# Performance work log

Hardware: AMD Instinct MI355X
Metric: run time of the kernel (lower is better)

## Reference

```python
import jax, jax.numpy as jnp
import numpy as np

NOISE_EPS = 0.01
TOP_K = 2


def setup_inputs() -> dict:
    key = jax.random.key(0)
    k1, k2, k3, k4 = jax.random.split(key, 4)
    B, S, D, E = 4, 4096, 2048, 64
    x = jax.random.normal(k1, (B, S, D), dtype=jnp.float32)
    raw_noise = jax.random.normal(k2, (B, S, E), dtype=jnp.float32)
    # gating_mlp: single Linear(D -> E), init std=0.02, zero bias
    W_gate = 0.02 * jax.random.normal(k3, (E, D), dtype=jnp.float32)
    b_gate = jnp.zeros((E,), dtype=jnp.float32)
    # noise_projection: Linear(D -> E, bias=False), init std=1/sqrt(D)
    W_noise = (1.0 / np.sqrt(D)) * jax.random.normal(k4, (E, D), dtype=jnp.float32)
    return {"x": x, "raw_noise": raw_noise, "W_gate": W_gate, "b_gate": b_gate, "W_noise": W_noise}


def reference(x, raw_noise, W_gate, b_gate, W_noise):
    # gate logits: [B,S,E]
    logits = jnp.einsum("bsd,ed->bse", x, W_gate) + b_gate
    # noisy top-k routing (training path)
    noise_stddev = jax.nn.softplus(jnp.einsum("bsd,ed->bse", x, W_noise)) + NOISE_EPS
    noisy = logits + raw_noise * noise_stddev
    top_v, top_i = jax.lax.top_k(noisy, TOP_K)            # [B,S,K]
    top_p = jax.nn.softmax(top_v.astype(jnp.float32), axis=-1).astype(noisy.dtype)
    B, S, E = noisy.shape
    T = B * S
    flat_logits = noisy.reshape(T, E)
    flat_i = top_i.reshape(T, TOP_K)
    flat_p = top_p.reshape(T, TOP_K)
    sparse = jnp.zeros((T, E), dtype=noisy.dtype).at[jnp.arange(T)[:, None], flat_i].set(flat_p)
    # aux load-balancing loss
    indicator = (sparse > 0.0).astype(jnp.float32)
    fraction_routed = indicator.sum(axis=0) / T           # f_e
    router_probs = jax.nn.softmax(flat_logits.astype(jnp.float32), axis=-1)
    avg_prob = router_probs.mean(axis=0)                  # p_e
    aux_loss = jnp.sum(fraction_routed * avg_prob) * E
    return sparse.reshape(B, S, E), aux_loss.astype(noisy.dtype)
```

## Files before the change

### kernel.cpp

```cpp
#include <hip/hip_runtime.h>
#include <math.h>

#define TOK 16384
#define DD  2048
#define EE  64
#define MT  32
#define BK  32
#define NKC 32
#define LDA 40

typedef _Float16 half4v __attribute__((ext_vector_type(4)));
typedef _Float16 half8  __attribute__((ext_vector_type(8)));
typedef float    floatx4 __attribute__((ext_vector_type(4)));

__global__ void build_wf(const float* __restrict__ Wg, const float* __restrict__ Wn,
                         _Float16* __restrict__ wf) {
  int tid  = blockIdx.x * 256 + threadIdx.x;
  int lane = tid & 63;
  int kc   = (tid >> 6) & 63;
  int ct   = tid >> 12;
  int col  = (ct & 3) * 16 + (lane & 15);
  int k    = kc * 32 + (lane >> 4) * 8;
  const float* W = (ct < 4) ? Wg : Wn;
  const float* src = W + (size_t)col * DD + k;
  float4 a = *reinterpret_cast<const float4*>(src);
  float4 b = *reinterpret_cast<const float4*>(src + 4);
  float v[8] = {a.x, a.y, a.z, a.w, b.x, b.y, b.z, b.w};
  half8 hi, lo;
#pragma unroll
  for (int j = 0; j < 8; ++j) {
    _Float16 h = (_Float16)v[j];
    hi[j] = h;
    lo[j] = (_Float16)(v[j] - (float)h);
  }
  size_t base = (((size_t)(ct * 64 + kc) * 2 + 0) * 64 + lane) * 8;
  *reinterpret_cast<half8*>(wf + base)       = hi;
  *reinterpret_cast<half8*>(wf + base + 512) = lo;
}

__global__ __launch_bounds__(512, 4)
void gating_kernel(const float* __restrict__ x, const float* __restrict__ rn,
                   const _Float16* __restrict__ wf, const float* __restrict__ bg,
                   float* __restrict__ out,
                   float* __restrict__ cnt_g, float* __restrict__ psum_g) {
  __shared__ char smem[33920];
  _Float16* xs   = (_Float16*)smem;
  float*    Pacc = (float*)smem;
  float*    Vb   = (float*)(smem + 16384);
  float*    Eb   = (float*)(smem + 24832);
  float*    isum = (float*)(smem + 33280);
  int*      ti   = (int*)(smem + 33408);
  float*    tp   = (float*)(smem + 33664);

  const int t  = threadIdx.x;
  const int g  = t >> 8;
  const int tg = t & 255;
  const int w4 = tg >> 6;
  const int l  = t & 63;
  const int q  = l >> 4;
  const int cl = l & 15;
  const int c  = w4 * 16 + cl;
  const int t0 = blockIdx.x * MT;

  const int stok = tg >> 3;
  const int skof = (tg & 7) * 4;
  const float* xrow = x + (size_t)(t0 + stok) * DD + g * (NKC * BK) + skof;

  float bgv = 0.f;
  float rnv[2][4] = {{0.f,0.f,0.f,0.f},{0.f,0.f,0.f,0.f}};
  if (g == 0) {
    bgv = bg[c];
#pragma unroll
    for (int mt = 0; mt < 2; ++mt)
#pragma unroll
      for (int r = 0; r < 4; ++r)
        rnv[mt][r] = rn[(size_t)(t0 + mt * 16 + q * 4 + r) * EE + c];
  }

  floatx4 acc[2][2];
#pragma unroll
  for (int mt = 0; mt < 2; ++mt)
#pragma unroll
    for (int nt = 0; nt < 2; ++nt) acc[mt][nt] = (floatx4)0.f;

  const half8* wfp = (const half8*)wf;
  half8 B[2][2][2];

  {
    float4 a = *reinterpret_cast<const float4*>(xrow);
    float v[4] = {a.x, a.y, a.z, a.w};
    half4v hi, lo;
#pragma unroll
    for (int j = 0; j < 4; ++j) {
      _Float16 h = (_Float16)v[j];
      hi[j] = h;
      lo[j] = (_Float16)(v[j] - (float)h);
    }
    *reinterpret_cast<half4v*>(&xs[((g * 2 + 0) * 2 + 0) * (MT * LDA) + stok * LDA + skof]) = hi;
    *reinterpret_cast<half4v*>(&xs[((g * 2 + 0) * 2 + 1) * (MT * LDA) + stok * LDA + skof]) = lo;
#pragma unroll
    for (int nt = 0; nt < 2; ++nt) {
      const int ct = w4 + nt * 4;
#pragma unroll
      for (int s = 0; s < 2; ++s)
        B[0][nt][s] = wfp[((size_t)(ct * 64 + g * NKC) * 2 + s) * 64 + l];
    }
  }

#pragma unroll 4
  for (int kc = 0; kc < NKC; ++kc) {
    const int cur = kc & 1;
    const bool more = (kc < NKC - 1);
    float4 pa;
    if (more) {
      pa = *reinterpret_cast<const float4*>(xrow + (kc + 1) * BK);
#pragma unroll
      for (int nt = 0; nt < 2; ++nt) {
        const int ct = w4 + nt * 4;
#pragma unroll
        for (int s = 0; s < 2; ++s)
          B[cur ^ 1][nt][s] = wfp[((size_t)(ct * 64 + g * NKC + kc + 1) * 2 + s) * 64 + l];
      }
    }
    asm volatile("s_waitcnt lgkmcnt(0)" ::: "memory");
    __builtin_amdgcn_s_barrier();

    half8 Ah[2], Al[2];
#pragma unroll
    for (int mt = 0; mt < 2; ++mt) {
      Ah[mt] = *reinterpret_cast<const half8*>(
          &xs[((g * 2 + cur) * 2 + 0) * (MT * LDA) + (mt * 16 + cl) * LDA + q * 8]);
      Al[mt] = *reinterpret_cast<const half8*>(
          &xs[((g * 2 + cur) * 2 + 1) * (MT * LDA) + (mt * 16 + cl) * LDA + q * 8]);
    }
#pragma unroll
    for (int mt = 0; mt < 2; ++mt)
#pragma unroll
      for (int nt = 0; nt < 2; ++nt)
        acc[mt][nt] = __builtin_amdgcn_mfma_f32_16x16x32_f16(Ah[mt], B[cur][nt][0], acc[mt][nt], 0, 0, 0);
#pragma unroll
    for (int mt = 0; mt < 2; ++mt)
#pragma unroll
      for (int nt = 0; nt < 2; ++nt)
        acc[mt][nt] = __builtin_amdgcn_mfma_f32_16x16x32_f16(Ah[mt], B[cur][nt][1], acc[mt][nt], 0, 0, 0);
#pragma unroll
    for (int mt = 0; mt < 2; ++mt)
#pragma unroll
      for (int nt = 0; nt < 2; ++nt)
        acc[mt][nt] = __builtin_amdgcn_mfma_f32_16x16x32_f16(Al[mt], B[cur][nt][0], acc[mt][nt], 0, 0, 0);

    if (more) {
      float v[4] = {pa.x, pa.y, pa.z, pa.w};
      half4v hi, lo;
#pragma unroll
      for (int j = 0; j < 4; ++j) {
        _Float16 h = (_Float16)v[j];
        hi[j] = h;
        lo[j] = (_Float16)(v[j] - (float)h);
      }
      *reinterpret_cast<half4v*>(&xs[((g * 2 + (cur ^ 1)) * 2 + 0) * (MT * LDA) + stok * LDA + skof]) = hi;
      *reinterpret_cast<half4v*>(&xs[((g * 2 + (cur ^ 1)) * 2 + 1) * (MT * LDA) + stok * LDA + skof]) = lo;
    }
  }

  __syncthreads();

  if (g == 1) {
#pragma unroll
    for (int mt = 0; mt < 2; ++mt)
#pragma unroll
      for (int nt = 0; nt < 2; ++nt)
#pragma unroll
        for (int r = 0; r < 4; ++r)
          Pacc[((((w4 * 2 + mt) * 2 + nt) * 4) + r) * 64 + l] = acc[mt][nt][r];
  }
  __syncthreads();

  if (g == 0) {
#pragma unroll
    for (int mt = 0; mt < 2; ++mt)
#pragma unroll
      for (int nt = 0; nt < 2; ++nt)
#pragma unroll
        for (int r = 0; r < 4; ++r)
          acc[mt][nt][r] += Pacc[((((w4 * 2 + mt) * 2 + nt) * 4) + r) * 64 + l];

#pragma unroll
    for (int mt = 0; mt < 2; ++mt)
#pragma unroll
      for (int r = 0; r < 4; ++r) {
        const int tk = mt * 16 + q * 4 + r;
        float gt = acc[mt][0][r] + bgv;
        float h  = acc[mt][1][r];
        float sp = (h > 20.f) ? h : log1pf(expf(h));
        float v  = gt + rnv[mt][r] * (sp + 0.01f);
        Vb[tk * 66 + c] = v;
        Eb[tk * 66 + c] = expf(v);
      }
  }
  __syncthreads();

  if (t < MT) {
    float v1 = -1e30f, v2 = -1e30f;
    int   i1 = 0, i2 = 0;
    float s = 0.f;
    for (int e = 0; e < EE; ++e) {
      float v = Vb[t * 66 + e];
      s += Eb[t * 66 + e];
      if (v > v1)      { v2 = v1; i2 = i1; v1 = v; i1 = e; }
      else if (v > v2) { v2 = v;  i2 = e; }
    }
    isum[t] = 1.f / s;
    ti[t * 2 + 0] = i1; ti[t * 2 + 1] = i2;
    float e2 = expf(v2 - v1);
    float dn = 1.f + e2;
    tp[t * 2 + 0] = 1.f / dn;
    tp[t * 2 + 1] = e2 / dn;
  }
  __syncthreads();

  {
    const int m  = t >> 4;
    const int c0 = (t & 15) * 4;
    const int i1 = ti[m * 2 + 0], i2 = ti[m * 2 + 1];
    const float p1 = tp[m * 2 + 0], p2 = tp[m * 2 + 1];
    float o[4];
#pragma unroll
    for (int j = 0; j < 4; ++j) {
      const int col = c0 + j;
      o[j] = (col == i1) ? p1 : ((col == i2) ? p2 : 0.f);
    }
    *reinterpret_cast<float4*>(out + (size_t)(t0 + m) * EE + c0) =
        make_float4(o[0], o[1], o[2], o[3]);
  }

  if (t < EE) {
    float s = 0.f;
    int   cn = 0;
#pragma unroll
    for (int m = 0; m < MT; ++m) {
      s  += Eb[m * 66 + t] * isum[m];
      cn += (ti[m * 2 + 0] == t) + (ti[m * 2 + 1] == t);
    }
    atomicAdd(&psum_g[t], s);
    atomicAdd(&cnt_g[t], (float)cn);
  }
}

__global__ void aux_kernel(const float* __restrict__ cnt_g,
                           const float* __restrict__ psum_g,
                           float* __restrict__ out) {
  int e = threadIdx.x;
  float v = cnt_g[e] * psum_g[e];
#pragma unroll
  for (int o = 32; o > 0; o >>= 1) v += __shfl_down(v, o);
  if (e == 0)
    out[(size_t)TOK * EE] = v * ((float)EE / ((float)TOK * (float)TOK));
}

extern "C" void kernel_launch(void* const* d_in, const int* in_sizes, int n_in,
                              void* d_out, int out_size, void* d_ws, size_t ws_size,
                              hipStream_t stream) {
  const float* x  = (const float*)d_in[0];
  const float* rn = (const float*)d_in[1];
  const float* Wg = (const float*)d_in[2];
  const float* bg = (const float*)d_in[3];
  const float* Wn = (const float*)d_in[4];
  float* out    = (float*)d_out;
  float* cnt_g  = (float*)d_ws;
  float* psum_g = cnt_g + EE;
  _Float16* wf  = (_Float16*)((float*)d_ws + 128);

  hipMemsetAsync(d_ws, 0, 2 * EE * sizeof(float), stream);
  build_wf<<<128, 256, 0, stream>>>(Wg, Wn, wf);
  gating_kernel<<<TOK / MT, 512, 0, stream>>>(x, rn, wf, bg, out, cnt_g, psum_g);
  aux_kernel<<<1, 64, 0, stream>>>(cnt_g, psum_g, out);
}
```

Measured before the change: 237.5 us.

## Stage four K-slices per barrier to cut synchronization in gating GEMM

Each outer iteration now stages a 128-wide K chunk of x (four 32-wide slices) into shared memory instead of one 32-wide slice, so there are 8 barriers per half-K instead of 32. Weight fragments are software-pipelined one sub-slice ahead with ping-pong registers, and more x loads are in flight per thread. Shared memory grows to about 68 KB per block, which can lower the number of resident blocks per CU and reduce occupancy.

```diff
diff --git a/kernel.cpp b/kernel.cpp
--- a/kernel.cpp
+++ b/kernel.cpp
@@ -5,9 +5,10 @@
 #define DD  2048
 #define EE  64
 #define MT  32
-#define BK  32
-#define NKC 32
-#define LDA 40
+#define BK  128
+#define NKC 8
+#define LDA 136
+#define XREG (MT * LDA)
 
 typedef _Float16 half4v __attribute__((ext_vector_type(4)));
 typedef _Float16 half8  __attribute__((ext_vector_type(8)));
@@ -38,12 +39,67 @@
   *reinterpret_cast<half8*>(wf + base + 512) = lo;
 }
 
+#define STAGE(BUF, P0, P1, P2, P3)                                              \
+  {                                                                             \
+    float4 pav[4] = {P0, P1, P2, P3};                                           \
+    _Float16* xh = xs + ((g * 2 + (BUF)) * 2 + 0) * XREG + stok * LDA + skof;   \
+    _Float16* xl = xh + XREG;                                                   \
+    _Pragma("unroll")                                                           \
+    for (int j = 0; j < 4; ++j) {                                               \
+      float v[4] = {pav[j].x, pav[j].y, pav[j].z, pav[j].w};                    \
+      half4v hi, lo;                                                            \
+      _Pragma("unroll")                                                         \
+      for (int jj = 0; jj < 4; ++jj) {                                          \
+        _Float16 h = (_Float16)v[jj];                                           \
+        hi[jj] = h;                                                             \
+        lo[jj] = (_Float16)(v[jj] - (float)h);                                  \
+      }                                                                         \
+      *reinterpret_cast<half4v*>(xh + j * 32) = hi;                             \
+      *reinterpret_cast<half4v*>(xl + j * 32) = lo;                             \
+    }                                                                           \
+  }
+
+#define SUBK(KK, SC, SP, DOPF)                                                  \
+  {                                                                             \
+    half8 Ah[2], Al[2];                                                         \
+    _Pragma("unroll")                                                           \
+    for (int mt = 0; mt < 2; ++mt) {                                            \
+      Ah[mt] = *reinterpret_cast<const half8*>(xsh + (mt * 16) * LDA + (KK) * 32); \
+      Al[mt] = *reinterpret_cast<const half8*>(xsl + (mt * 16) * LDA + (KK) * 32); \
+    }                                                                           \
+    if (DOPF) {                                                                 \
+      const int ck = g * 32 + kc * 4 + (KK) + 1;                                \
+      _Pragma("unroll")                                                         \
+      for (int nt = 0; nt < 2; ++nt) {                                          \
+        const int ct = w4 + nt * 4;                                             \
+        _Pragma("unroll")                                                       \
+        for (int s = 0; s < 2; ++s)                                             \
+          SP[nt][s] = wfp[((size_t)(ct * 64 + ck) * 2 + s) * 64 + l];           \
+      }                                                                         \
+    }                                                                           \
+    _Pragma("unroll")                                                           \
+    for (int mt = 0; mt < 2; ++mt)                                              \
+      _Pragma("unroll")                                                         \
+      for (int nt = 0; nt < 2; ++nt)                                            \
+        acc[mt][nt] = __builtin_amdgcn_mfma_f32_16x16x32_f16(Ah[mt], SC[nt][0], acc[mt][nt], 0, 0, 0); \
+    _Pragma("unroll")                                                           \
+    for (int mt = 0; mt < 2; ++mt)                                              \
+      _Pragma("unroll")                                                         \
+      for (int nt = 0; nt < 2; ++nt)                                            \
+        acc[mt][nt] = __builtin_amdgcn_mfma_f32_16x16x32_f16(Ah[mt], SC[nt][1], acc[mt][nt], 0, 0, 0); \
+    _Pragma("unroll")                                                           \
+    for (int mt = 0; mt < 2; ++mt)                                              \
+      _Pragma("unroll")                                                         \
+      for (int nt = 0; nt < 2; ++nt)                                            \
+        acc[mt][nt] = __builtin_amdgcn_mfma_f32_16x16x32_f16(Al[mt], SC[nt][0], acc[mt][nt], 0, 0, 0); \
+  }
+
 __global__ __launch_bounds__(512, 4)
 void gating_kernel(const float* __restrict__ x, const float* __restrict__ rn,
                    const _Float16* __restrict__ wf, const float* __restrict__ bg,
                    float* __restrict__ out,
                    float* __restrict__ cnt_g, float* __restrict__ psum_g) {
-  __shared__ char smem[33920];
+  __shared__ char smem[69632];
   _Float16* xs   = (_Float16*)smem;
   float*    Pacc = (float*)smem;
   float*    Vb   = (float*)(smem + 16384);
@@ -84,82 +140,49 @@
     for (int nt = 0; nt < 2; ++nt) acc[mt][nt] = (floatx4)0.f;
 
   const half8* wfp = (const half8*)wf;
-  half8 B[2][2][2];
+  half8 Bs0[2][2], Bs1[2][2];
 
   {
-    float4 a = *reinterpret_cast<const float4*>(xrow);
-    float v[4] = {a.x, a.y, a.z, a.w};
-    half4v hi, lo;
-#pragma unroll
-    for (int j = 0; j < 4; ++j) {
-      _Float16 h = (_Float16)v[j];
-      hi[j] = h;
-      lo[j] = (_Float16)(v[j] - (float)h);
-    }
-    *reinterpret_cast<half4v*>(&xs[((g * 2 + 0) * 2 + 0) * (MT * LDA) + stok * LDA + skof]) = hi;
-    *reinterpret_cast<half4v*>(&xs[((g * 2 + 0) * 2 + 1) * (MT * LDA) + stok * LDA + skof]) = lo;
+    float4 a0 = *reinterpret_cast<const float4*>(xrow);
+    float4 a1 = *reinterpret_cast<const float4*>(xrow + 32);
+    float4 a2 = *reinterpret_cast<const float4*>(xrow + 64);
+    float4 a3 = *reinterpret_cast<const float4*>(xrow + 96);
+    STAGE(0, a0, a1, a2, a3)
+    const int ck0 = g * 32;
 #pragma unroll
     for (int nt = 0; nt < 2; ++nt) {
       const int ct = w4 + nt * 4;
 #pragma unroll
       for (int s = 0; s < 2; ++s)
-        B[0][nt][s] = wfp[((size_t)(ct * 64 + g * NKC) * 2 + s) * 64 + l];
-    }
-  }
-
-#pragma unroll 4
+        Bs0[nt][s] = wfp[((size_t)(ct * 64 + ck0) * 2 + s) * 64 + l];
+    }
+  }
+
+#pragma unroll 2
   for (int kc = 0; kc < NKC; ++kc) {
     const int cur = kc & 1;
     const bool more = (kc < NKC - 1);
-    float4 pa;
+    float4 p0, p1, p2, p3;
     if (more) {
-      pa = *reinterpret_cast<const float4*>(xrow + (kc + 1) * BK);
-#pragma unroll
-      for (int nt = 0; nt < 2; ++nt) {
-        const int ct = w4 + nt * 4;
-#pragma unroll
-        for (int s = 0; s < 2; ++s)
-          B[cur ^ 1][nt][s] = wfp[((size_t)(ct * 64 + g * NKC + kc + 1) * 2 + s) * 64 + l];
-      }
+      const float* xn = xrow + (kc + 1) * BK;
+      p0 = *reinterpret_cast<const float4*>(xn);
+      p1 = *reinterpret_cast<const float4*>(xn + 32);
+      p2 = *reinterpret_cast<const float4*>(xn + 64);
+      p3 = *reinterpret_cast<const float4*>(xn + 96);
     }
     asm volatile("s_waitcnt lgkmcnt(0)" ::: "memory");
     __builtin_amdgcn_s_barrier();
 
-    half8 Ah[2], Al[2];
-#pragma unroll
-    for (int mt = 0; mt < 2; ++mt) {
-      Ah[mt] = *reinterpret_cast<const half8*>(
-          &xs[((g * 2 + cur) * 2 + 0) * (MT * LDA) + (mt * 16 + cl) * LDA + q * 8]);
-      Al[mt] = *reinterpret_cast<const half8*>(
-          &xs[((g * 2 + cur) * 2 + 1) * (MT * LDA) + (mt * 16 + cl) * LDA + q * 8]);
-    }
-#pragma unroll
-    for (int mt = 0; mt < 2; ++mt)
-#pragma unroll
-      for (int nt = 0; nt < 2; ++nt)
-        acc[mt][nt] = __builtin_amdgcn_mfma_f32_16x16x32_f16(Ah[mt], B[cur][nt][0], acc[mt][nt], 0, 0, 0);
-#pragma unroll
-    for (int mt = 0; mt < 2; ++mt)
-#pragma unroll
-      for (int nt = 0; nt < 2; ++nt)
-        acc[mt][nt] = __builtin_amdgcn_mfma_f32_16x16x32_f16(Ah[mt], B[cur][nt][1], acc[mt][nt], 0, 0, 0);
-#pragma unroll
-    for (int mt = 0; mt < 2; ++mt)
-#pragma unroll
-      for (int nt = 0; nt < 2; ++nt)
-        acc[mt][nt] = __builtin_amdgcn_mfma_f32_16x16x32_f16(Al[mt], B[cur][nt][0], acc[mt][nt], 0, 0, 0);
+    const _Float16* xsh = xs + ((g * 2 + cur) * 2 + 0) * XREG + cl * LDA + q * 8;
+    const _Float16* xsl = xsh + XREG;
+
+    SUBK(0, Bs0, Bs1, 1)
+    SUBK(1, Bs1, Bs0, 1)
+    SUBK(2, Bs0, Bs1, 1)
+    SUBK(3, Bs1, Bs0, more)
 
     if (more) {
-      float v[4] = {pa.x, pa.y, pa.z, pa.w};
-      half4v hi, lo;
-#pragma unroll
-      for (int j = 0; j < 4; ++j) {
-        _Float16 h = (_Float16)v[j];
-        hi[j] = h;
-        lo[j] = (_Float16)(v[j] - (float)h);
-      }
-      *reinterpret_cast<half4v*>(&xs[((g * 2 + (cur ^ 1)) * 2 + 0) * (MT * LDA) + stok * LDA + skof]) = hi;
-      *reinterpret_cast<half4v*>(&xs[((g * 2 + (cur ^ 1)) * 2 + 1) * (MT * LDA) + stok * LDA + skof]) = lo;
+      STAGE(cur ^ 1, p0, p1, p2, p3)
     }
   }
 
```

New measurement: 226.9 us. 4.5% less time.
